# Optimization experiments

Measured on AMD Instinct MI355X. Metric: run time of the kernel, lower is better.

The kernel has to match this reference:

```python
import jax, jax.numpy as jnp
import numpy as np

DIM = 1024
DIM_LATENT = 1024
DIM_HEAD = 64
INNER = max(DIM, DIM_LATENT)  # 1024
HEADS = INNER // DIM_HEAD     # 16
SCALE = DIM_HEAD ** -0.5
LN_EPS = 1e-5
RMS_EPS = 1e-8


def layernorm(x, g, b):
    mu = jnp.mean(x, axis=-1, keepdims=True)
    var = jnp.mean(jnp.square(x - mu), axis=-1, keepdims=True)
    return (x - mu) * jax.lax.rsqrt(var + LN_EPS) * g + b


def rmsnorm(x, gamma):
    # torch: x / clamp(norm(x,-1) * d**-0.5, eps) * gamma
    n = jnp.linalg.norm(x, axis=-1, keepdims=True) * (x.shape[-1] ** -0.5)
    return x / jnp.maximum(n, RMS_EPS) * gamma


def setup_inputs() -> dict:
    key = jax.random.key(0)
    ks = jax.random.split(key, 8)
    b, n, nl = 8, 2048, 512
    x = jax.random.normal(ks[0], (b, n, DIM), dtype=jnp.float32)
    latents = jax.random.normal(ks[1], (b, nl, DIM_LATENT), dtype=jnp.float32)
    mask = jax.random.randint(ks[2], (b, n), 0, 2).astype(bool)
    init = lambda k, shape, fan_in: jax.random.normal(k, shape, jnp.float32) * (fan_in ** -0.5)
    return {
        "x": x,
        "latents": latents,
        "mask": mask,
        "ln_x_g": jnp.ones((DIM,), jnp.float32),
        "ln_x_b": jnp.zeros((DIM,), jnp.float32),
        "ln_l_g": jnp.ones((DIM_LATENT,), jnp.float32),
        "ln_l_b": jnp.zeros((DIM_LATENT,), jnp.float32),
        "q_gamma": jnp.ones((DIM_HEAD,), jnp.float32),
        "k_gamma": jnp.ones((DIM_HEAD,), jnp.float32),
        "W_q": init(ks[3], (DIM_LATENT, INNER), DIM_LATENT),
        "W_kv": init(ks[4], (DIM, 2 * INNER), DIM),
        "W_out": init(ks[5], (INNER, DIM_LATENT), INNER),
        "b_out": jnp.zeros((DIM_LATENT,), jnp.float32),
    }


def reference(x, latents, mask, ln_x_g, ln_x_b, ln_l_g, ln_l_b,
              q_gamma, k_gamma, W_q, W_kv, W_out, b_out):
    b, n, _ = x.shape
    nl = latents.shape[1]
    xn = layernorm(x, ln_x_g, ln_x_b)
    ln = layernorm(latents, ln_l_g, ln_l_b)

    q = ln @ W_q                                   # [b, nl, inner]
    kv = jnp.concatenate([xn @ W_kv, ln @ W_kv], axis=1)  # [b, n+nl, 2*inner]
    k, v = kv[..., :INNER], kv[..., INNER:]

    to_heads = lambda t: t.reshape(t.shape[0], t.shape[1], HEADS, DIM_HEAD).transpose(0, 2, 1, 3)
    q, k, v = to_heads(q), to_heads(k), to_heads(v)  # [b, h, *, d]

    qn = rmsnorm(q, q_gamma) * SCALE
    kn = rmsnorm(k, k_gamma)

    sim = jnp.einsum('bhid,bhjd->bhij', qn, kn)      # [b, h, nl, n+nl]
    full_mask = jnp.pad(mask, ((0, 0), (0, nl)), constant_values=True)
    neg = -jnp.finfo(sim.dtype).max
    sim = jnp.where(full_mask[:, None, None, :], sim, neg)

    attn = jax.nn.softmax(sim.astype(jnp.float32), axis=-1).astype(sim.dtype)
    out = jnp.einsum('bhij,bhjd->bhid', attn, v)     # [b, h, nl, d]
    out = out.transpose(0, 2, 1, 3).reshape(b, nl, INNER)
    return out @ W_out + b_out
```

## Files before the change

### kernel.cpp

```cpp
#include <hip/hip_runtime.h>
#include <hip/hip_bf16.h>
#include <cfloat>
#include <cmath>

typedef __hip_bfloat16 bf16;
#define DEV_INLINE __device__ __forceinline__

typedef __attribute__((ext_vector_type(8))) short short8;
typedef __attribute__((ext_vector_type(4))) short short4v;
typedef __attribute__((ext_vector_type(4))) float float4v;
typedef __attribute__((ext_vector_type(16))) float float16v;

#define BATCH 8
#define NSEQ 2048
#define NLAT 512
#define DIM_ 1024
#define NKV 2560
#define HEADS_ 16
#define DHEAD 64
#define SCALE_ 0.125f
#define LN_EPS_ 1e-5f
#define RMS_EPS_ 1e-8f

DEV_INLINE float bf2f(bf16 v) { return __bfloat162float(v); }
DEV_INLINE bf16 f2bf(float v) { return __float2bfloat16(v); }
DEV_INLINE short bfbits(float x) { union { bf16 b; short s; } c; c.b = f2bf(x); return c.s; }
DEV_INLINE float sbits2f(short s) { union { bf16 b; short s; } c; c.s = s; return bf2f(c.b); }

DEV_INLINE int detect_bf16(const void* ones) {
    return (*(const unsigned*)ones == 0x3F803F80u) ? 1 : 0;
}

template<typename T> DEV_INLINE float ldf(const T* p);
template<> DEV_INLINE float ldf<float>(const float* p) { return *p; }
template<> DEV_INLINE float ldf<bf16>(const bf16* p)  { return __bfloat162float(*p); }

template<typename T> DEV_INLINE void ld4(const T* p, float* d);
template<> DEV_INLINE void ld4<float>(const float* p, float* d) {
    float4 f = *(const float4*)p;
    d[0] = f.x; d[1] = f.y; d[2] = f.z; d[3] = f.w;
}
template<> DEV_INLINE void ld4<bf16>(const bf16* p, float* d) {
    short4v s = *(const short4v*)p;
    #pragma unroll
    for (int j = 0; j < 4; j++) d[j] = sbits2f(s[j]);
}

DEV_INLINE void gload16(const bf16* g, bf16* l) {
    __builtin_amdgcn_global_load_lds(
        (const __attribute__((address_space(1))) unsigned int*)g,
        (__attribute__((address_space(3))) unsigned int*)l,
        16, 0, 0);
}

template<typename T>
DEV_INLINE void ln_rows_wave(int r, const void* xv, const void* latv,
                             const void* gxv, const void* bxv,
                             const void* glv, const void* blv,
                             bf16* __restrict__ out)
{
    const T* src; const T* g; const T* be; bf16* o;
    if (r < BATCH * NSEQ) {
        int b = r >> 11, i = r & 2047;
        src = (const T*)xv + (size_t)r * DIM_;
        o = out + ((size_t)b * NKV + i) * DIM_;
        g = (const T*)gxv; be = (const T*)bxv;
    } else {
        int rr = r - BATCH * NSEQ;
        int b = rr >> 9, i = rr & 511;
        src = (const T*)latv + (size_t)rr * DIM_;
        o = out + ((size_t)b * NKV + NSEQ + i) * DIM_;
        g = (const T*)glv; be = (const T*)blv;
    }
    int lane = threadIdx.x & 63;
    float v[16];
    #pragma unroll
    for (int k = 0; k < 4; k++) ld4(src + k * 256 + lane * 4, &v[k * 4]);
    float s = 0.f, s2 = 0.f;
    #pragma unroll
    for (int j = 0; j < 16; j++) { s += v[j]; s2 += v[j] * v[j]; }
    #pragma unroll
    for (int off = 1; off < 64; off <<= 1) {
        s  += __shfl_xor(s, off, 64);
        s2 += __shfl_xor(s2, off, 64);
    }
    float mu = s * (1.f / 1024.f);
    float var = fmaxf(s2 * (1.f / 1024.f) - mu * mu, 0.f);
    float rstd = rsqrtf(var + LN_EPS_);
    #pragma unroll
    for (int k = 0; k < 4; k++) {
        float gv[4], bv[4];
        ld4(g + k * 256 + lane * 4, gv);
        ld4(be + k * 256 + lane * 4, bv);
        short4v ov;
        #pragma unroll
        for (int j = 0; j < 4; j++)
            ov[j] = bfbits((v[k * 4 + j] - mu) * rstd * gv[j] + bv[j]);
        *(short4v*)(o + k * 256 + lane * 4) = ov;
    }
}

template<typename T>
DEV_INLINE void trans_body(int bid, const void* wqv, const void* wkvv, const void* woutv,
                           bf16* wqT, bf16* wkvT, bf16* woutT, float* tile )
{
    const T* in; bf16* out; int N, t0;
    if (bid < 1024)      { in = (const T*)wqv;   out = wqT;   N = 1024; t0 = bid; }
    else if (bid < 3072) { in = (const T*)wkvv;  out = wkvT;  N = 2048; t0 = bid - 1024; }
    else                 { in = (const T*)woutv; out = woutT; N = 1024; t0 = bid - 3072; }
    int K = 1024;
    int nb = N >> 5;
    int bn = (t0 % nb) * 32, bk = (t0 / nb) * 32;
    int tx = threadIdx.x & 31, ty = threadIdx.x >> 5;
    #pragma unroll
    for (int j = 0; j < 4; j++)
        tile[(ty + j * 8) * 33 + tx] = ldf(in + (size_t)(bk + ty + j * 8) * N + bn + tx);
    __syncthreads();
    #pragma unroll
    for (int j = 0; j < 4; j++)
        out[(size_t)(bn + ty + j * 8) * K + bk + tx] = f2bf(tile[tx * 33 + ty + j * 8]);
}

__global__ __launch_bounds__(256) void prep_kernel(
    const void* x, const void* lat,
    const void* gx, const void* bx, const void* gl, const void* bl,
    const void* wq, const void* wkv, const void* wout,
    bf16* __restrict__ cat_n, bf16* __restrict__ wqT,
    bf16* __restrict__ wkvT, bf16* __restrict__ woutT)
{
    __shared__ float smem[32 * 33];
    int isb = detect_bf16(gx);
    int bid = blockIdx.x;
    if (bid < 5120) {
        int r = bid * 4 + (threadIdx.x >> 6);
        if (isb) ln_rows_wave<bf16>(r, x, lat, gx, bx, gl, bl, cat_n);
        else     ln_rows_wave<float>(r, x, lat, gx, bx, gl, bl, cat_n);
    } else {
        int t = bid - 5120;
        if (isb) trans_body<bf16>(t, wq, wkv, wout, wqT, wkvT, woutT, smem);
        else     trans_body<float>(t, wq, wkv, wout, wqT, wkvT, woutT, smem);
    }
}

#define MFMA_CORE_128(As, Bs, Apt, Bpt, K, acc)                                \
    {                                                                          \
        bf16* Asl_ = &As[threadIdx.x * 8];                                     \
        bf16* Bsl_ = &Bs[threadIdx.x * 8];                                     \
        for (int k0 = 0; k0 < K; k0 += 64) {                                   \
            __syncthreads();                                                   \
            _Pragma("unroll")                                                  \
            for (int rep = 0; rep < 4; rep++) {                                \
                gload16(Apt[rep] + k0, Asl_ + rep * 2048);                     \
                gload16(Bpt[rep] + k0, Bsl_ + rep * 2048);                     \
            }                                                                  \
            __syncthreads();                                                   \
            _Pragma("unroll")                                                  \
            for (int kk = 0; kk < 4; kk++) {                                   \
                short8 af_[2], bf_[2];                                         \
                _Pragma("unroll")                                              \
                for (int ms = 0; ms < 2; ms++) {                               \
                    int row = wm * 64 + ms * 32 + l32;                         \
                    int jc = (kk * 2 + h5) ^ (row & 7);                        \
                    af_[ms] = *(const short8*)&As[row * 64 + jc * 8];          \
                }                                                              \
                _Pragma("unroll")                                              \
                for (int ns = 0; ns < 2; ns++) {                               \
                    int row = wn * 64 + ns * 32 + l32;                         \
                    int jc = (kk * 2 + h5) ^ (row & 7);                        \
                    bf_[ns] = *(const short8*)&Bs[row * 64 + jc * 8];          \
                }                                                              \
                _Pragma("unroll")                                              \
                for (int ms = 0; ms < 2; ms++)                                 \
                    _Pragma("unroll")                                          \
                    for (int ns = 0; ns < 2; ns++)                             \
                        acc[ms][ns] = __builtin_amdgcn_mfma_f32_32x32x16_bf16( \
                            af_[ms], bf_[ns], acc[ms][ns], 0, 0, 0);           \
            }                                                                  \
        }                                                                      \
    }

#define QKV_MFMA2(BQ0, BQ1, NB)                                               \
    __builtin_amdgcn_s_barrier(); asm volatile("" ::: "memory");              \
    __builtin_amdgcn_s_setprio(1);                                            \
    _Pragma("unroll")                                                         \
    for (int m_ = 0; m_ < 8; m_++) {                                          \
        acc[m_][NB] = __builtin_amdgcn_mfma_f32_16x16x32_bf16(                \
            af[m_], BQ0, acc[m_][NB], 0, 0, 0);                               \
        acc[m_][NB + 1] = __builtin_amdgcn_mfma_f32_16x16x32_bf16(            \
            af[m_], BQ1, acc[m_][NB + 1], 0, 0, 0);                           \
    }                                                                         \
    __builtin_amdgcn_s_setprio(0);                                            \
    __builtin_amdgcn_s_barrier(); asm volatile("" ::: "memory");

__global__ __launch_bounds__(512, 2) void gemm_qkv(
    const void* gq, const void* gk,
    const bf16* __restrict__ cat_n, const bf16* __restrict__ wkvT,
    const bf16* __restrict__ wqT,
    bf16* __restrict__ kbuf, bf16* __restrict__ vtbuf, bf16* __restrict__ qbuf)
{
    __shared__ bf16 S[8][8192];
    int isb = detect_bf16(gq);
    int tid = threadIdx.x;
    int bid = blockIdx.x;
    int lane = tid & 63;
    int l16 = lane & 15, quad = lane >> 4;
    int wv = tid >> 6;
    int wm = wv >> 2, wn = wv & 3;

    int x = bid & 7, ii = bid >> 3;
    int bm, bn; bool isq; const bf16* Bt;
    if (ii < 80) { bm = (ii >> 3) * 8 + x; bn = ii & 7; Bt = wkvT; isq = false; }
    else { int j = ii - 80; bm = (j >> 2) * 8 + x; bn = j & 3; Bt = wqT; isq = true; }

    int r0 = tid >> 2;
    int c0 = (tid & 3) ^ ((r0 >> 1) & 3);
    int r1 = (tid + 512) >> 2;
    int c1 = (tid & 3) ^ ((r1 >> 1) & 3);
    int ar0 = bm * 256 + r0, ar1 = bm * 256 + r1;
    size_t ga0 = isq ? ((size_t)(ar0 >> 9) * NKV + NSEQ + (ar0 & 511)) : (size_t)ar0;
    size_t ga1 = isq ? ((size_t)(ar1 >> 9) * NKV + NSEQ + (ar1 & 511)) : (size_t)ar1;
    const bf16* pA0 = cat_n + ga0 * 1024 + c0 * 8;
    const bf16* pA1 = cat_n + ga1 * 1024 + c1 * 8;
    const bf16* pB0 = Bt + (size_t)(bn * 256 + r0) * 1024 + c0 * 8;
    const bf16* pB1 = Bt + (size_t)(bn * 256 + r1) * 1024 + c1 * 8;

#define STG(P0, P1, SLOT, KO) do {                                            \
        gload16((P0) + (KO), &S[SLOT][0] + tid * 8);                          \
        gload16((P1) + (KO), &S[SLOT][0] + 4096 + tid * 8);                   \
    } while (0)

    int qx = (quad ^ ((l16 >> 1) & 3)) * 8;
    int aoff = (wm * 128 + l16) * 32 + qx;
    int boff = (wn * 64 + l16) * 32 + qx;

    float4v acc[8][4];
    #pragma unroll
    for (int m = 0; m < 8; m++)
        #pragma unroll
        for (int n = 0; n < 4; n++)
            #pragma unroll
            for (int r = 0; r < 4; r++) acc[m][n][r] = 0.f;

    STG(pA0, pA1, 0, 0);
    STG(pB0, pB1, 2, 0);
    STG(pA0, pA1, 1, 32);
    STG(pB0, pB1, 3, 32);
    STG(pA0, pA1, 4, 64);
    STG(pB0, pB1, 6, 64);
    asm volatile("s_waitcnt vmcnt(4)" ::: "memory");
    __builtin_amdgcn_s_barrier(); asm volatile("" ::: "memory");

    short8 af[8], b0[4], b1[4];
    b0[0] = *(const short8*)&S[2][boff];
    b0[1] = *(const short8*)&S[2][boff + 512];

    for (int t = 0; t < 16; ++t) {
        int cur = (t & 1) * 4, nxt = cur ^ 4;
        const bf16* A0k = &S[cur + 0][0];
        const bf16* A1k = &S[cur + 1][0];
        const bf16* B0k = &S[cur + 2][0];
        const bf16* B1k = &S[cur + 3][0];
        const bf16* Bn0 = &S[nxt + 2][0];
        int ko1 = t * 64 + 96;
        int ko2 = t * 64 + 128;

        #pragma unroll
        for (int m = 0; m < 8; m++) af[m] = *(const short8*)&A0k[aoff + m * 512];
        if (t < 15) STG(pA0, pA1, nxt + 1, ko1);
        QKV_MFMA2(b0[0], b0[1], 0)

        b0[2] = *(const short8*)&B0k[boff + 1024];
        b0[3] = *(const short8*)&B0k[boff + 1536];
        b1[0] = *(const short8*)&B1k[boff];
        b1[1] = *(const short8*)&B1k[boff + 512];
        if (t < 15) STG(pB0, pB1, nxt + 3, ko1);
        QKV_MFMA2(b0[2], b0[3], 2)

        #pragma unroll
        for (int m = 0; m < 8; m++) af[m] = *(const short8*)&A1k[aoff + m * 512];
        if (t < 14) STG(pA0, pA1, cur + 0, ko2);
        QKV_MFMA2(b1[0], b1[1], 0)

        b1[2] = *(const short8*)&B1k[boff + 1024];
        b1[3] = *(const short8*)&B1k[boff + 1536];
        if (t < 14) {
            STG(pB0, pB1, cur + 2, ko2);
            asm volatile("s_waitcnt vmcnt(4)" ::: "memory");
        } else {
            asm volatile("s_waitcnt vmcnt(0)" ::: "memory");
        }
        if (t < 15) {
            b0[0] = *(const short8*)&Bn0[boff];
            b0[1] = *(const short8*)&Bn0[boff + 512];
        }
        QKV_MFMA2(b1[2], b1[3], 2)
    }
#undef STG

    if (isq || bn < 4) {
        const void* gp = isq ? gq : gk;
        float g2[4];
        #pragma unroll
        for (int n = 0; n < 4; n++) {
            int idx = n * 16 + l16;
            g2[n] = isb ? bf2f(((const bf16*)gp)[idx]) : ((const float*)gp)[idx];
        }
        #pragma unroll
        for (int m = 0; m < 8; m++) {
            #pragma unroll
            for (int r = 0; r < 4; r++) {
                float ss = acc[m][0][r] * acc[m][0][r]
                         + acc[m][1][r] * acc[m][1][r]
                         + acc[m][2][r] * acc[m][2][r]
                         + acc[m][3][r] * acc[m][3][r];
                ss += __shfl_xor(ss, 1, 64);
                ss += __shfl_xor(ss, 2, 64);
                ss += __shfl_xor(ss, 4, 64);
                ss += __shfl_xor(ss, 8, 64);
                float nn = sqrtf(ss) * 0.125f;
                float inv = 1.0f / fmaxf(nn, RMS_EPS_);
                if (isq) inv *= SCALE_;
                #pragma unroll
                for (int n = 0; n < 4; n++) acc[m][n][r] *= inv * g2[n];
            }
        }
    }

    if (!isq && bn >= 4) {
        int bq_ = bm / 10;
        int key0 = (bm % 10) * 256 + wm * 128;
        #pragma unroll
        for (int m = 0; m < 8; m++) {
            int key = key0 + m * 16 + quad * 4;
            #pragma unroll
            for (int n = 0; n < 4; n++) {
                int col = bn * 256 + wn * 64 + n * 16 + l16 - 1024;
                int h = col >> 6, d = col & 63;
                short4v ov;
                #pragma unroll
                for (int r = 0; r < 4; r++) ov[r] = bfbits(acc[m][n][r]);
                *(short4v*)(vtbuf + ((size_t)((bq_ * 16 + h) * 64 + d)) * NKV + key) = ov;
            }
        }
    } else {
        bf16* C = isq ? qbuf : kbuf;
        int rbase = bm * 256 + wm * 128;
        int cbase = bn * 256 + wn * 64;
        #pragma unroll
        for (int m = 0; m < 8; m++) {
            #pragma unroll
            for (int r = 0; r < 4; r++) {
                int row = rbase + m * 16 + quad * 4 + r;
                #pragma unroll
                for (int n = 0; n < 4; n++)
                    C[(size_t)row * 1024 + cbase + n * 16 + l16] = f2bf(acc[m][n][r]);
            }
        }
    }
}

#define KC 64
__global__ __launch_bounds__(256) void attn_mfma(
    const bf16* __restrict__ q, const bf16* __restrict__ kbuf,
    const bf16* __restrict__ vtbuf, const int* __restrict__ maskp,
    const void* gk, bf16* __restrict__ out)
{
    __shared__ bf16 Ks[KC * 64];
    __shared__ bf16 Vt[DHEAD * 64];
    __shared__ bf16 Ps[4][2][16][64];
    __shared__ float msk_s[KC];

    int isb = detect_bf16(gk);
    int tid = threadIdx.x;
    int bid = blockIdx.x;
    int bh = bid & 127, qb = bid >> 7;
    int h = bh & 15, bb = bh >> 4;
    int wv = tid >> 6, lane = tid & 63, quad = lane >> 4, l16 = lane & 15;
    int q8 = quad * 8;
    int qbase = qb * 128 + wv * 32;
    int sw = l16 & 7;

    const bf16* kbase = kbuf + (size_t)bb * NKV * 1024 + h * DHEAD;
    const bf16* vbase = vtbuf + (size_t)(bb * 16 + h) * DHEAD * NKV;

    short8 qf[2][2];
    #pragma unroll
    for (int qt = 0; qt < 2; qt++) {
        const bf16* qp = q + ((size_t)(bb * NLAT + qbase + qt * 16 + l16)) * 1024 + h * DHEAD;
        qf[qt][0] = *(const short8*)(qp + q8);
        qf[qt][1] = *(const short8*)(qp + q8 + 32);
    }

    float gv = isb ? bf2f(((const bf16*)gk)[lane]) : ((const float*)gk)[lane];
    gv = fabsf(gv);
    #pragma unroll
    for (int o = 1; o < 64; o <<= 1) gv = fmaxf(gv, __shfl_xor(gv, o, 64));
    float m_fix[2];
    #pragma unroll
    for (int qt = 0; qt < 2; qt++) {
        float ssq = 0.f;
        #pragma unroll
        for (int j = 0; j < 8; j++) {
            float a = sbits2f(qf[qt][0][j]);
            float b = sbits2f(qf[qt][1][j]);
            ssq += a * a + b * b;
        }
        ssq += __shfl_xor(ssq, 16, 64);
        ssq += __shfl_xor(ssq, 32, 64);
        m_fix[qt] = sqrtf(ssq) * 8.0f * gv;
    }

    int c0 = tid, c1 = tid + 256;
    int krow0 = c0 >> 3, kj0 = ((c0 & 7) ^ (krow0 & 7)) * 8;
    int krow1 = c1 >> 3, kj1 = ((c1 & 7) ^ (krow1 & 7)) * 8;

    float4v o_acc[2][4];
    #pragma unroll
    for (int qt = 0; qt < 2; qt++)
        #pragma unroll
        for (int ds = 0; ds < 4; ds++)
            #pragma unroll
            for (int r = 0; r < 4; r++) o_acc[qt][ds][r] = 0.f;
    float l_i[2] = {0.f, 0.f};

    for (int kb = 0; kb < NKV; kb += KC) {
        __syncthreads();
        gload16(kbase + (size_t)(kb + krow0) * 1024 + kj0, &Ks[c0 * 8]);
        gload16(kbase + (size_t)(kb + krow1) * 1024 + kj1, &Ks[c1 * 8]);
        gload16(vbase + (size_t)krow0 * NKV + kb + kj0, &Vt[c0 * 8]);
        gload16(vbase + (size_t)krow1 * NKV + kb + kj1, &Vt[c1 * 8]);
        if (tid < KC) {
            int key = kb + tid;
            float mv = 0.f;
            if (key < NSEQ) mv = maskp[bb * NSEQ + key] ? 0.f : -1e30f;
            msk_s[tid] = mv;
        }
        __syncthreads();

        float4v st[2][4];
        #pragma unroll
        for (int kt = 0; kt < 4; kt++) {
            int row = kt * 16 + l16;
            short8 kf0 = *(const short8*)&Ks[row * 64 + ((quad ^ sw) << 3)];
            short8 kf1 = *(const short8*)&Ks[row * 64 + (((quad + 4) ^ sw) << 3)];
            #pragma unroll
            for (int qt = 0; qt < 2; qt++) {
                float4v z; z[0]=0.f; z[1]=0.f; z[2]=0.f; z[3]=0.f;
                z = __builtin_amdgcn_mfma_f32_16x16x32_bf16(kf0, qf[qt][0], z, 0, 0, 0);
                z = __builtin_amdgcn_mfma_f32_16x16x32_bf16(kf1, qf[qt][1], z, 0, 0, 0);
                st[qt][kt] = z;
            }
        }
        float4 mv4[4];
        #pragma unroll
        for (int kt = 0; kt < 4; kt++) mv4[kt] = *(const float4*)&msk_s[kt * 16 + 4 * quad];
        #pragma unroll
        for (int qt = 0; qt < 2; qt++) {
            float lp = 0.f;
            #pragma unroll
            for (int kt = 0; kt < 4; kt++) {
                const float* mk = (const float*)&mv4[kt];
                short4v pk;
                #pragma unroll
                for (int r = 0; r < 4; r++) {
                    float e = __expf(st[qt][kt][r] + mk[r] - m_fix[qt]);
                    lp += e;
                    pk[r] = bfbits(e);
                }
                int j = kt * 2 + (quad >> 1);
                int js = j ^ sw;
                *(short4v*)&Ps[wv][qt][l16][js * 8 + (quad & 1) * 4] = pk;
            }
            l_i[qt] += lp;
        }

        #pragma unroll
        for (int kc = 0; kc < 2; kc++) {
            short8 pf[2];
            #pragma unroll
            for (int qt = 0; qt < 2; qt++)
                pf[qt] = *(const short8*)&Ps[wv][qt][l16][((kc * 4 + quad) ^ sw) * 8];
            #pragma unroll
            for (int ds = 0; ds < 4; ds++) {
                int row = ds * 16 + l16;
                short8 vf = *(const short8*)&Vt[row * 64 + (((kc * 4 + quad) ^ sw) << 3)];
                #pragma unroll
                for (int qt = 0; qt < 2; qt++)
                    o_acc[qt][ds] = __builtin_amdgcn_mfma_f32_16x16x32_bf16(vf, pf[qt], o_acc[qt][ds], 0, 0, 0);
            }
        }
    }

    #pragma unroll
    for (int qt = 0; qt < 2; qt++) {
        float l = l_i[qt];
        l += __shfl_xor(l, 16, 64);
        l += __shfl_xor(l, 32, 64);
        float inv = 1.0f / l;
        bf16* op = out + ((size_t)(bb * NLAT + qbase + qt * 16 + l16)) * 1024 + h * DHEAD;
        #pragma unroll
        for (int ds = 0; ds < 4; ds++) {
            short4v ov;
            #pragma unroll
            for (int r = 0; r < 4; r++) ov[r] = bfbits(o_acc[qt][ds][r] * inv);
            *(short4v*)(op + ds * 16 + 4 * quad) = ov;
        }
    }
}

__global__ __launch_bounds__(256) void gemm_out(
    const void* ones, const void* bias,
    const bf16* __restrict__ A, const bf16* __restrict__ Bt, void* __restrict__ Cout)
{
    __shared__ bf16 As[128 * 64];
    __shared__ bf16 Bs[128 * 64];
    int isb = detect_bf16(ones);

    int tid = threadIdx.x;
    int bid = blockIdx.x;
    int bm = (bid >> 6) * 8 + (bid & 7);
    int bn = (bid >> 3) & 7;
    int wv = tid >> 6, lane = tid & 63, l32 = lane & 31, h5 = lane >> 5;
    int wm = wv >> 1, wn = wv & 1;
    const int K = 1024, N = 1024;

    const bf16* Apt[4]; const bf16* Bpt[4];
    #pragma unroll
    for (int rep = 0; rep < 4; rep++) {
        int c = rep * 256 + tid;
        int row = c >> 3;
        int k8 = ((c & 7) ^ (row & 7)) * 8;
        Apt[rep] = A + (size_t)(bm * 128 + row) * K + k8;
        Bpt[rep] = Bt + (size_t)(bn * 128 + row) * K + k8;
    }

    float16v acc[2][2];
    #pragma unroll
    for (int i = 0; i < 2; i++)
        #pragma unroll
        for (int j = 0; j < 2; j++)
            #pragma unroll
            for (int r = 0; r < 16; r++) acc[i][j][r] = 0.f;

    MFMA_CORE_128(As, Bs, Apt, Bpt, K, acc);

    #pragma unroll
    for (int ms = 0; ms < 2; ms++) {
        #pragma unroll
        for (int rg = 0; rg < 4; rg++) {
            int row0 = bm * 128 + wm * 64 + ms * 32 + rg * 8 + h5 * 4;
            #pragma unroll
            for (int rr = 0; rr < 4; rr++) {
                int row = row0 + rr;
                #pragma unroll
                for (int ns = 0; ns < 2; ns++) {
                    int col = bn * 128 + wn * 64 + ns * 32 + l32;
                    float bv = isb ? bf2f(((const bf16*)bias)[col]) : ((const float*)bias)[col];
                    float v = acc[ms][ns][rg * 4 + rr] + bv;
                    if (isb) ((bf16*)Cout)[(size_t)row * N + col] = f2bf(v);
                    else     ((float*)Cout)[(size_t)row * N + col] = v;
                }
            }
        }
    }
}

extern "C" void kernel_launch(void* const* d_in, const int* in_sizes, int n_in,
                              void* d_out, int out_size, void* d_ws, size_t ws_size,
                              hipStream_t stream) {
    const int* mask = (const int*)d_in[2];

    char* ws = (char*)d_ws;
    size_t off = 0;
    bf16* cat_n   = (bf16*)(ws + off); off += (size_t)20480 * 1024 * 2;
    bf16* kbuf    = (bf16*)(ws + off); off += (size_t)20480 * 1024 * 2;
    bf16* vtbuf   = (bf16*)(ws + off); off += (size_t)8192 * 2560 * 2;
    bf16* qbuf    = (bf16*)(ws + off); off += (size_t)4096 * 1024 * 2;
    bf16* attnout = (bf16*)(ws + off); off += (size_t)4096 * 1024 * 2;
    bf16* wqT     = (bf16*)(ws + off); off += (size_t)1024 * 1024 * 2;
    bf16* wkvT    = (bf16*)(ws + off); off += (size_t)2048 * 1024 * 2;
    bf16* woutT   = (bf16*)(ws + off); off += (size_t)1024 * 1024 * 2;

    prep_kernel<<<9216, 256, 0, stream>>>(
        d_in[0], d_in[1], d_in[3], d_in[4], d_in[5], d_in[6],
        d_in[9], d_in[10], d_in[11], cat_n, wqT, wkvT, woutT);

    gemm_qkv<<<704, 512, 0, stream>>>(
        d_in[7], d_in[8], cat_n, wkvT, wqT, kbuf, vtbuf, qbuf);

    attn_mfma<<<512, 256, 0, stream>>>(qbuf, kbuf, vtbuf, mask, d_in[8], attnout);

    gemm_out<<<256, 256, 0, stream>>>(
        d_in[3], d_in[12], attnout, woutT, d_out);
}
```

Measured before the change: 359.6 us.

## Double-buffer K/V tiles in attention and preload full mask to LDS

The attention kernel now keeps two LDS buffers for K and V tiles. It issues loads for the next tile before computing on the current one, and uses one barrier per iteration instead of two. The per-batch mask is converted once into an LDS array covering all keys, instead of being reloaded for every tile. This is meant to hide global load latency behind the MFMA and softmax work, at the cost of more LDS, which may reduce occupancy. Whether it is correct depends on gload16 being a synchronous register-staged copy, or on proper waits being in place.

```diff
diff --git a/kernel.cpp b/kernel.cpp
--- a/kernel.cpp
+++ b/kernel.cpp
@@ -365,10 +365,10 @@
     const bf16* __restrict__ vtbuf, const int* __restrict__ maskp,
     const void* gk, bf16* __restrict__ out)
 {
-    __shared__ bf16 Ks[KC * 64];
-    __shared__ bf16 Vt[DHEAD * 64];
+    __shared__ bf16 Ks[2][KC * 64];
+    __shared__ bf16 Vt[2][DHEAD * 64];
     __shared__ bf16 Ps[4][2][16][64];
-    __shared__ float msk_s[KC];
+    __shared__ float msk_all[NSEQ];
 
     int isb = detect_bf16(gk);
     int tid = threadIdx.x;
@@ -383,6 +383,12 @@
     const bf16* kbase = kbuf + (size_t)bb * NKV * 1024 + h * DHEAD;
     const bf16* vbase = vtbuf + (size_t)(bb * 16 + h) * DHEAD * NKV;
 
+    #pragma unroll
+    for (int j = 0; j < 8; j++) {
+        int key = j * 256 + tid;
+        msk_all[key] = maskp[bb * NSEQ + key] ? 0.f : -1e30f;
+    }
+
     short8 qf[2][2];
     #pragma unroll
     for (int qt = 0; qt < 2; qt++) {
@@ -414,6 +420,13 @@
     int krow0 = c0 >> 3, kj0 = ((c0 & 7) ^ (krow0 & 7)) * 8;
     int krow1 = c1 >> 3, kj1 = ((c1 & 7) ^ (krow1 & 7)) * 8;
 
+#define ASTG(B, KB) do {                                                      \
+        gload16(kbase + (size_t)((KB) + krow0) * 1024 + kj0, &Ks[B][c0 * 8]); \
+        gload16(kbase + (size_t)((KB) + krow1) * 1024 + kj1, &Ks[B][c1 * 8]); \
+        gload16(vbase + (size_t)krow0 * NKV + (KB) + kj0, &Vt[B][c0 * 8]);    \
+        gload16(vbase + (size_t)krow1 * NKV + (KB) + kj1, &Vt[B][c1 * 8]);    \
+    } while (0)
+
     float4v o_acc[2][4];
     #pragma unroll
     for (int qt = 0; qt < 2; qt++)
@@ -423,26 +436,19 @@
             for (int r = 0; r < 4; r++) o_acc[qt][ds][r] = 0.f;
     float l_i[2] = {0.f, 0.f};
 
+    ASTG(0, 0);
+    __syncthreads();
+
+    int buf = 0;
     for (int kb = 0; kb < NKV; kb += KC) {
-        __syncthreads();
-        gload16(kbase + (size_t)(kb + krow0) * 1024 + kj0, &Ks[c0 * 8]);
-        gload16(kbase + (size_t)(kb + krow1) * 1024 + kj1, &Ks[c1 * 8]);
-        gload16(vbase + (size_t)krow0 * NKV + kb + kj0, &Vt[c0 * 8]);
-        gload16(vbase + (size_t)krow1 * NKV + kb + kj1, &Vt[c1 * 8]);
-        if (tid < KC) {
-            int key = kb + tid;
-            float mv = 0.f;
-            if (key < NSEQ) mv = maskp[bb * NSEQ + key] ? 0.f : -1e30f;
-            msk_s[tid] = mv;
-        }
-        __syncthreads();
+        if (kb + KC < NKV) ASTG(buf ^ 1, kb + KC);
 
         float4v st[2][4];
         #pragma unroll
         for (int kt = 0; kt < 4; kt++) {
             int row = kt * 16 + l16;
-            short8 kf0 = *(const short8*)&Ks[row * 64 + ((quad ^ sw) << 3)];
-            short8 kf1 = *(const short8*)&Ks[row * 64 + (((quad + 4) ^ sw) << 3)];
+            short8 kf0 = *(const short8*)&Ks[buf][row * 64 + ((quad ^ sw) << 3)];
+            short8 kf1 = *(const short8*)&Ks[buf][row * 64 + (((quad + 4) ^ sw) << 3)];
             #pragma unroll
             for (int qt = 0; qt < 2; qt++) {
                 float4v z; z[0]=0.f; z[1]=0.f; z[2]=0.f; z[3]=0.f;
@@ -452,8 +458,15 @@
             }
         }
         float4 mv4[4];
-        #pragma unroll
-        for (int kt = 0; kt < 4; kt++) mv4[kt] = *(const float4*)&msk_s[kt * 16 + 4 * quad];
+        if (kb < NSEQ) {
+            #pragma unroll
+            for (int kt = 0; kt < 4; kt++)
+                mv4[kt] = *(const float4*)&msk_all[kb + kt * 16 + 4 * quad];
+        } else {
+            #pragma unroll
+            for (int kt = 0; kt < 4; kt++)
+                mv4[kt] = make_float4(0.f, 0.f, 0.f, 0.f);
+        }
         #pragma unroll
         for (int qt = 0; qt < 2; qt++) {
             float lp = 0.f;
@@ -483,13 +496,17 @@
             #pragma unroll
             for (int ds = 0; ds < 4; ds++) {
                 int row = ds * 16 + l16;
-                short8 vf = *(const short8*)&Vt[row * 64 + (((kc * 4 + quad) ^ sw) << 3)];
+                short8 vf = *(const short8*)&Vt[buf][row * 64 + (((kc * 4 + quad) ^ sw) << 3)];
                 #pragma unroll
                 for (int qt = 0; qt < 2; qt++)
                     o_acc[qt][ds] = __builtin_amdgcn_mfma_f32_16x16x32_bf16(vf, pf[qt], o_acc[qt][ds], 0, 0, 0);
             }
         }
-    }
+
+        __syncthreads();
+        buf ^= 1;
+    }
+#undef ASTG
 
     #pragma unroll
     for (int qt = 0; qt < 2; qt++) {
```

Result: no change. 363.7 us (+1.1%).
